# Performance work log

Measured on AMD Instinct MI355X. Metric: run time of the kernel, lower is better.

Reference implementation:

```python
import jax, jax.numpy as jnp
import numpy as np

N, D, C = 2048, 192, 100000
S, M = 30.0, 0.2

def setup_inputs() -> dict:
    key = jax.random.key(0)
    k1, k2, k3 = jax.random.split(key, 3)
    x = jax.random.normal(k1, (N, D), dtype=jnp.float32)
    W = jax.random.normal(k2, (C, D), dtype=jnp.float32) * 0.05
    label = jax.random.randint(k3, (N,), 0, C, dtype=jnp.int64)
    return {"x": x, "W": W, "label": label}

def reference(x, W, label):
    # NOTE: the original torch code's weight-normalization loop is a no-op
    # (it rebinds the local name W, never mutating the parameter), so W is
    # intentionally NOT normalized here; only x is.
    xn = x / jnp.linalg.norm(x, axis=1, keepdims=True)          # [N, D]
    wf = jnp.einsum("nd,cd->nc", xn, W)                          # [N, C]
    tgt = jnp.take_along_axis(wf, label[:, None], axis=1)[:, 0]  # [N]
    numer = S * (tgt - M)                                        # margin-adjusted target logit
    logits = S * wf
    # replace the label column with the margin-adjusted numerator so that
    # logsumexp(logits) == log(exp(numer) + sum_{j!=y} exp(s*wf[:,j]))
    logits = logits.at[jnp.arange(N), label].set(numer)
    L = numer - jax.nn.logsumexp(logits, axis=1)                 # [N]
    return -jnp.mean(L)
```

## Files before the change

kernel.cpp:

```cpp
#include <hip/hip_runtime.h>
#include <stdint.h>


constexpr int N  = 2048;
constexpr int D  = 192;
constexpr int C  = 100000;
constexpr int KT = D / 32;
constexpr int TILE = 512;
constexpr int RT16 = C / 16;
constexpr int TPG = 12;
constexpr int CX = 523;
constexpr int RY = 16;
constexpr int NT16 = CX * TPG;
constexpr float PHANTOM = (float)(NT16 * 16 - C);

#define S_SCALE 30.0f
#define MARGIN  0.2f
#define S_LOG2E 43.2808512266689f

using short8 = __attribute__((ext_vector_type(8))) short;
using f32x4  = __attribute__((ext_vector_type(4))) float;

typedef __attribute__((address_space(1))) const void GV;
typedef __attribute__((address_space(3))) void LV;

__device__ inline unsigned short f2bf(float f) {
  unsigned int u = __float_as_uint(f);
  u += 0x7fffu + ((u >> 16) & 1u);
  return (unsigned short)(u >> 16);
}

__device__ inline int pack_idx(int r, int k) {
  return ((r >> 4) * KT + (k >> 5)) * TILE + (((k >> 3) & 3) * 16 + (r & 15)) * 8 + (k & 7);
}

__device__ inline float row_sum16(float v) {
  int x;
  x = __float_as_int(v);
  v += __int_as_float(__builtin_amdgcn_update_dpp(0, x, 0x128, 0xF, 0xF, true));
  x = __float_as_int(v);
  v += __int_as_float(__builtin_amdgcn_update_dpp(0, x, 0x124, 0xF, 0xF, true));
  x = __float_as_int(v);
  v += __int_as_float(__builtin_amdgcn_update_dpp(0, x, 0x04E, 0xF, 0xF, true));
  x = __float_as_int(v);
  v += __int_as_float(__builtin_amdgcn_update_dpp(0, x, 0x0B1, 0xF, 0xF, true));
  return v;
}

__global__ __launch_bounds__(256) void prep_x(const float* __restrict__ x,
                                              unsigned short* __restrict__ xnb) {
  const int row  = blockIdx.x * 4 + (threadIdx.x >> 6);
  const int lane = threadIdx.x & 63;
  const float* xr = x + (size_t)row * D;
  float v0 = xr[lane], v1 = xr[lane + 64], v2 = xr[lane + 128];
  float ss = v0 * v0 + v1 * v1 + v2 * v2;
#pragma unroll
  for (int off = 32; off > 0; off >>= 1) ss += __shfl_xor(ss, off, 64);
  const float inv = rsqrtf(ss) * S_LOG2E;
  xnb[pack_idx(row, lane)]       = f2bf(v0 * inv);
  xnb[pack_idx(row, lane + 64)]  = f2bf(v1 * inv);
  xnb[pack_idx(row, lane + 128)] = f2bf(v2 * inv);
}

__global__ __launch_bounds__(256) void prep_w(const float* __restrict__ W,
                                              unsigned short* __restrict__ Wb) {
  const int t16  = blockIdx.x * 4 + (threadIdx.x >> 6);
  const int lane = threadIdx.x & 63;
  const int m = lane & 15, q = lane >> 4;
  unsigned short* dst = Wb + (size_t)t16 * KT * TILE + lane * 8;
  if (t16 < RT16) {
    const float* src = W + (size_t)(t16 * 16 + m) * D + q * 8;
#pragma unroll
    for (int ks = 0; ks < KT; ++ks) {
      const float4* s4 = (const float4*)(src + ks * 32);
      float4 f0 = s4[0], f1 = s4[1];
      short8 hv;
      hv[0] = (short)f2bf(f0.x); hv[1] = (short)f2bf(f0.y);
      hv[2] = (short)f2bf(f0.z); hv[3] = (short)f2bf(f0.w);
      hv[4] = (short)f2bf(f1.x); hv[5] = (short)f2bf(f1.y);
      hv[6] = (short)f2bf(f1.z); hv[7] = (short)f2bf(f1.w);
      *(short8*)(dst + (size_t)ks * TILE) = hv;
    }
  } else {
    const short8 z = {0, 0, 0, 0, 0, 0, 0, 0};
#pragma unroll
    for (int ks = 0; ks < KT; ++ks) *(short8*)(dst + (size_t)ks * TILE) = z;
  }
}

__global__ __launch_bounds__(256, 3) void gemm_lse(
    const unsigned short* __restrict__ xnb,
    const unsigned short* __restrict__ Wb,
    float* __restrict__ partial) {
  __shared__ alignas(16) unsigned short As[8 * KT * TILE];
  __shared__ alignas(16) float rs_lds[4][128];

  const int tid = threadIdx.x;
  const int bid = blockIdx.x;
  const int cx = bid >> 4, ry = bid & 15;

  const unsigned short* slab = xnb + (size_t)(ry * 8) * KT * TILE;
#pragma unroll
  for (int i = 0; i < 12; ++i) {
    const int chunk = tid + i * 256;
    __builtin_amdgcn_global_load_lds(
        (GV*)((const char*)slab + (size_t)chunk * 16),
        (LV*)((char*)As + (size_t)chunk * 16), 16, 0, 0);
  }

  const int lane = tid & 63, wave = tid >> 6;
  const int m = lane & 15, quad = lane >> 4;

  short8 breg[3][KT];
#pragma unroll
  for (int tc = 0; tc < 3; ++tc)
#pragma unroll
    for (int ks = 0; ks < KT; ++ks)
      breg[tc][ks] = *(const short8*)(
          Wb + (size_t)((cx * TPG + wave * 3 + tc) * KT + ks) * TILE + lane * 8);

  __syncthreads();

  const f32x4 zero4 = {0.0f, 0.0f, 0.0f, 0.0f};

  for (int rs = 0; rs < 2; ++rs) {
    f32x4 acc[4][3];
#pragma unroll
    for (int a = 0; a < 4; ++a)
#pragma unroll
      for (int b = 0; b < 3; ++b) acc[a][b] = zero4;

#pragma unroll
    for (int ks = 0; ks < KT; ++ks) {
      short8 af[4];
#pragma unroll
      for (int tr = 0; tr < 4; ++tr)
        af[tr] = *(const short8*)(
            &As[((rs * 4 + tr) * KT + ks) * TILE + lane * 8]);
#pragma unroll
      for (int tr = 0; tr < 4; ++tr)
#pragma unroll
        for (int tc = 0; tc < 3; ++tc)
          acc[tr][tc] = __builtin_amdgcn_mfma_f32_16x16x32_bf16(
              af[tr], breg[tc][ks], acc[tr][tc], 0, 0, 0);
    }

#pragma unroll
    for (int tr = 0; tr < 4; ++tr) {
      float rv0 = 0.f, rv1 = 0.f, rv2 = 0.f, rv3 = 0.f;
#pragma unroll
      for (int tc = 0; tc < 3; ++tc) {
        rv0 += __builtin_amdgcn_exp2f(acc[tr][tc][0]);
        rv1 += __builtin_amdgcn_exp2f(acc[tr][tc][1]);
        rv2 += __builtin_amdgcn_exp2f(acc[tr][tc][2]);
        rv3 += __builtin_amdgcn_exp2f(acc[tr][tc][3]);
      }
      rv0 = row_sum16(rv0);
      rv1 = row_sum16(rv1);
      rv2 = row_sum16(rv2);
      rv3 = row_sum16(rv3);
      if (m == 0) {
        float4 v = make_float4(rv0, rv1, rv2, rv3);
        *(float4*)(&rs_lds[wave][rs * 64 + tr * 16 + quad * 4]) = v;
      }
    }
  }

  __syncthreads();
  if (tid < 128) {
    const float s = rs_lds[0][tid] + rs_lds[1][tid] + rs_lds[2][tid] + rs_lds[3][tid];
    partial[(size_t)cx * N + ry * 128 + tid] = s;
  }
}

__global__ __launch_bounds__(256) void finalize_rows(
    const float* __restrict__ x, const float* __restrict__ W,
    const int* __restrict__ label, const float* __restrict__ partial,
    float* __restrict__ Lrow) {
  const int row  = blockIdx.x * 4 + (threadIdx.x >> 6);
  const int lane = threadIdx.x & 63;
  const float* xr = x + (size_t)row * D;
  float v0 = xr[lane], v1 = xr[lane + 64], v2 = xr[lane + 128];
  float ss = v0 * v0 + v1 * v1 + v2 * v2;
  const int lab = label[row];
  const float* wr = W + (size_t)lab * D;
  float d = v0 * wr[lane] + v1 * wr[lane + 64] + v2 * wr[lane + 128];
  float p = 0.0f;
  for (int s = lane; s < CX; s += 64) p += partial[(size_t)s * N + row];
#pragma unroll
  for (int off = 32; off > 0; off >>= 1) {
    ss += __shfl_xor(ss, off, 64);
    d  += __shfl_xor(d,  off, 64);
    p  += __shfl_xor(p,  off, 64);
  }
  if (lane == 0) {
    const float tgt   = d * rsqrtf(ss);
    const float numer = S_SCALE * (tgt - MARGIN);
    const float se = p - PHANTOM - __expf(S_SCALE * tgt) + __expf(numer);
    Lrow[row] = numer - logf(se);
  }
}

__global__ __launch_bounds__(256) void reduce_loss(const float* __restrict__ Lrow,
                                                   float* __restrict__ out) {
  const int tid = threadIdx.x;
  float s = 0.0f;
  for (int i = tid; i < N; i += 256) s += Lrow[i];
#pragma unroll
  for (int off = 32; off > 0; off >>= 1) s += __shfl_xor(s, off, 64);
  __shared__ float part[4];
  if ((tid & 63) == 0) part[tid >> 6] = s;
  __syncthreads();
  if (tid == 0) out[0] = -(part[0] + part[1] + part[2] + part[3]) / (float)N;
}

extern "C" void kernel_launch(void* const* d_in, const int* in_sizes, int n_in,
                              void* d_out, int out_size, void* d_ws, size_t ws_size,
                              hipStream_t stream) {
  const float* x     = (const float*)d_in[0];
  const float* W     = (const float*)d_in[1];
  const int*   label = (const int*)d_in[2];
  float*       out   = (float*)d_out;

  char* ws = (char*)d_ws;
  size_t off = 0;
  unsigned short* xnb = (unsigned short*)(ws + off); off += (size_t)N * D * 2;
  unsigned short* Wb  = (unsigned short*)(ws + off); off += (size_t)NT16 * KT * TILE * 2;
  float* partial = (float*)(ws + off); off += (size_t)CX * N * 4;
  float* Lrow    = (float*)(ws + off);

  prep_x<<<N / 4, 256, 0, stream>>>(x, xnb);
  prep_w<<<NT16 / 4, 256, 0, stream>>>(W, Wb);

  gemm_lse<<<CX * RY, 256, 0, stream>>>(xnb, Wb, partial);

  finalize_rows<<<N / 4, 256, 0, stream>>>(x, W, label, partial, Lrow);
  reduce_loss<<<1, 256, 0, stream>>>(Lrow, out);
}
```

Measured before the change: 214.5 us.

## Double-buffer x bands in GEMM-LSE, merge prep kernels, fuse final reduction

Each gemm_lse block now covers 256 rows in four bands of 64 instead of 128 rows. That halves the number of blocks that reload the same W tiles into registers. The next x band is streamed into a second LDS buffer while the current band is being multiplied. The two prep kernels are merged into one launch, which also zeroes the output. The separate reduce kernel is replaced by per-block atomicAdd in finalize_rows. This trades fewer launches and less W reloading for fewer, longer blocks (1/8 of the grid is now per-cx), a larger LDS footprint, and an order-dependent float atomic sum.

```diff
diff --git a/kernel.cpp b/kernel.cpp
--- a/kernel.cpp
+++ b/kernel.cpp
@@ -10,9 +10,12 @@
 constexpr int RT16 = C / 16;
 constexpr int TPG = 12;
 constexpr int CX = 523;
-constexpr int RY = 16;
 constexpr int NT16 = CX * TPG;
 constexpr float PHANTOM = (float)(NT16 * 16 - C);
+constexpr int BANDS = 4;
+constexpr int RYB = N / (64 * BANDS);
+constexpr int BUF = 4 * KT * TILE;
+constexpr int NXB = N / 4;
 
 #define S_SCALE 30.0f
 #define MARGIN  0.2f
@@ -47,44 +50,47 @@
   return v;
 }
 
-__global__ __launch_bounds__(256) void prep_x(const float* __restrict__ x,
-                                              unsigned short* __restrict__ xnb) {
-  const int row  = blockIdx.x * 4 + (threadIdx.x >> 6);
+__global__ __launch_bounds__(256) void prep_all(
+    const float* __restrict__ x, const float* __restrict__ W,
+    unsigned short* __restrict__ xnb, unsigned short* __restrict__ Wb,
+    float* __restrict__ out) {
+  const int bid  = blockIdx.x;
   const int lane = threadIdx.x & 63;
-  const float* xr = x + (size_t)row * D;
-  float v0 = xr[lane], v1 = xr[lane + 64], v2 = xr[lane + 128];
-  float ss = v0 * v0 + v1 * v1 + v2 * v2;
-#pragma unroll
-  for (int off = 32; off > 0; off >>= 1) ss += __shfl_xor(ss, off, 64);
-  const float inv = rsqrtf(ss) * S_LOG2E;
-  xnb[pack_idx(row, lane)]       = f2bf(v0 * inv);
-  xnb[pack_idx(row, lane + 64)]  = f2bf(v1 * inv);
-  xnb[pack_idx(row, lane + 128)] = f2bf(v2 * inv);
-}
-
-__global__ __launch_bounds__(256) void prep_w(const float* __restrict__ W,
-                                              unsigned short* __restrict__ Wb) {
-  const int t16  = blockIdx.x * 4 + (threadIdx.x >> 6);
-  const int lane = threadIdx.x & 63;
-  const int m = lane & 15, q = lane >> 4;
-  unsigned short* dst = Wb + (size_t)t16 * KT * TILE + lane * 8;
-  if (t16 < RT16) {
-    const float* src = W + (size_t)(t16 * 16 + m) * D + q * 8;
-#pragma unroll
-    for (int ks = 0; ks < KT; ++ks) {
-      const float4* s4 = (const float4*)(src + ks * 32);
-      float4 f0 = s4[0], f1 = s4[1];
-      short8 hv;
-      hv[0] = (short)f2bf(f0.x); hv[1] = (short)f2bf(f0.y);
-      hv[2] = (short)f2bf(f0.z); hv[3] = (short)f2bf(f0.w);
-      hv[4] = (short)f2bf(f1.x); hv[5] = (short)f2bf(f1.y);
-      hv[6] = (short)f2bf(f1.z); hv[7] = (short)f2bf(f1.w);
-      *(short8*)(dst + (size_t)ks * TILE) = hv;
-    }
+  if (bid == 0 && threadIdx.x == 0) out[0] = 0.0f;
+
+  if (bid < NXB) {
+    const int row = bid * 4 + (threadIdx.x >> 6);
+    const float* xr = x + (size_t)row * D;
+    float v0 = xr[lane], v1 = xr[lane + 64], v2 = xr[lane + 128];
+    float ss = v0 * v0 + v1 * v1 + v2 * v2;
+#pragma unroll
+    for (int off = 32; off > 0; off >>= 1) ss += __shfl_xor(ss, off, 64);
+    const float inv = rsqrtf(ss) * S_LOG2E;
+    xnb[pack_idx(row, lane)]       = f2bf(v0 * inv);
+    xnb[pack_idx(row, lane + 64)]  = f2bf(v1 * inv);
+    xnb[pack_idx(row, lane + 128)] = f2bf(v2 * inv);
   } else {
-    const short8 z = {0, 0, 0, 0, 0, 0, 0, 0};
-#pragma unroll
-    for (int ks = 0; ks < KT; ++ks) *(short8*)(dst + (size_t)ks * TILE) = z;
+    const int t16 = (bid - NXB) * 4 + (threadIdx.x >> 6);
+    const int m = lane & 15, q = lane >> 4;
+    unsigned short* dst = Wb + (size_t)t16 * KT * TILE + lane * 8;
+    if (t16 < RT16) {
+      const float* src = W + (size_t)(t16 * 16 + m) * D + q * 8;
+#pragma unroll
+      for (int ks = 0; ks < KT; ++ks) {
+        const float4* s4 = (const float4*)(src + ks * 32);
+        float4 f0 = s4[0], f1 = s4[1];
+        short8 hv;
+        hv[0] = (short)f2bf(f0.x); hv[1] = (short)f2bf(f0.y);
+        hv[2] = (short)f2bf(f0.z); hv[3] = (short)f2bf(f0.w);
+        hv[4] = (short)f2bf(f1.x); hv[5] = (short)f2bf(f1.y);
+        hv[6] = (short)f2bf(f1.z); hv[7] = (short)f2bf(f1.w);
+        *(short8*)(dst + (size_t)ks * TILE) = hv;
+      }
+    } else {
+      const short8 z = {0, 0, 0, 0, 0, 0, 0, 0};
+#pragma unroll
+      for (int ks = 0; ks < KT; ++ks) *(short8*)(dst + (size_t)ks * TILE) = z;
+    }
   }
 }
 
@@ -92,20 +98,22 @@
     const unsigned short* __restrict__ xnb,
     const unsigned short* __restrict__ Wb,
     float* __restrict__ partial) {
-  __shared__ alignas(16) unsigned short As[8 * KT * TILE];
-  __shared__ alignas(16) float rs_lds[4][128];
+  __shared__ alignas(16) unsigned short As[2 * BUF];
+  __shared__ alignas(16) float rs_lds[4][256];
 
   const int tid = threadIdx.x;
   const int bid = blockIdx.x;
-  const int cx = bid >> 4, ry = bid & 15;
-
-  const unsigned short* slab = xnb + (size_t)(ry * 8) * KT * TILE;
-#pragma unroll
-  for (int i = 0; i < 12; ++i) {
-    const int chunk = tid + i * 256;
-    __builtin_amdgcn_global_load_lds(
-        (GV*)((const char*)slab + (size_t)chunk * 16),
-        (LV*)((char*)As + (size_t)chunk * 16), 16, 0, 0);
+  const int cx = bid >> 3, ry = bid & 7;
+
+  {
+    const unsigned short* slab = xnb + (size_t)(ry * BANDS) * BUF;
+#pragma unroll
+    for (int i = 0; i < 6; ++i) {
+      const int chunk = tid + i * 256;
+      __builtin_amdgcn_global_load_lds(
+          (GV*)((const char*)slab + (size_t)chunk * 16),
+          (LV*)((char*)As + (size_t)chunk * 16), 16, 0, 0);
+    }
   }
 
   const int lane = tid & 63, wave = tid >> 6;
@@ -119,24 +127,37 @@
       breg[tc][ks] = *(const short8*)(
           Wb + (size_t)((cx * TPG + wave * 3 + tc) * KT + ks) * TILE + lane * 8);
 
-  __syncthreads();
-
   const f32x4 zero4 = {0.0f, 0.0f, 0.0f, 0.0f};
 
-  for (int rs = 0; rs < 2; ++rs) {
+  for (int b = 0; b < BANDS; ++b) {
+    __syncthreads();
+
+    if (b + 1 < BANDS) {
+      const unsigned short* slab = xnb + (size_t)(ry * BANDS + b + 1) * BUF;
+      char* dst = (char*)&As[((b + 1) & 1) * BUF];
+#pragma unroll
+      for (int i = 0; i < 6; ++i) {
+        const int chunk = tid + i * 256;
+        __builtin_amdgcn_global_load_lds(
+            (GV*)((const char*)slab + (size_t)chunk * 16),
+            (LV*)(dst + (size_t)chunk * 16), 16, 0, 0);
+      }
+    }
+
+    const unsigned short* Ab = &As[(b & 1) * BUF];
+
     f32x4 acc[4][3];
 #pragma unroll
     for (int a = 0; a < 4; ++a)
 #pragma unroll
-      for (int b = 0; b < 3; ++b) acc[a][b] = zero4;
+      for (int c = 0; c < 3; ++c) acc[a][c] = zero4;
 
 #pragma unroll
     for (int ks = 0; ks < KT; ++ks) {
       short8 af[4];
 #pragma unroll
       for (int tr = 0; tr < 4; ++tr)
-        af[tr] = *(const short8*)(
-            &As[((rs * 4 + tr) * KT + ks) * TILE + lane * 8]);
+        af[tr] = *(const short8*)(&Ab[(tr * KT + ks) * TILE + lane * 8]);
 #pragma unroll
       for (int tr = 0; tr < 4; ++tr)
 #pragma unroll
@@ -161,22 +182,22 @@
       rv3 = row_sum16(rv3);
       if (m == 0) {
         float4 v = make_float4(rv0, rv1, rv2, rv3);
-        *(float4*)(&rs_lds[wave][rs * 64 + tr * 16 + quad * 4]) = v;
+        *(float4*)(&rs_lds[wave][b * 64 + tr * 16 + quad * 4]) = v;
       }
     }
   }
 
   __syncthreads();
-  if (tid < 128) {
+  if (tid < 256) {
     const float s = rs_lds[0][tid] + rs_lds[1][tid] + rs_lds[2][tid] + rs_lds[3][tid];
-    partial[(size_t)cx * N + ry * 128 + tid] = s;
+    partial[(size_t)cx * N + ry * 256 + tid] = s;
   }
 }
 
 __global__ __launch_bounds__(256) void finalize_rows(
     const float* __restrict__ x, const float* __restrict__ W,
     const int* __restrict__ label, const float* __restrict__ partial,
-    float* __restrict__ Lrow) {
+    float* __restrict__ out) {
   const int row  = blockIdx.x * 4 + (threadIdx.x >> 6);
   const int lane = threadIdx.x & 63;
   const float* xr = x + (size_t)row * D;
@@ -193,25 +214,18 @@
     d  += __shfl_xor(d,  off, 64);
     p  += __shfl_xor(p,  off, 64);
   }
+  __shared__ float part[4];
   if (lane == 0) {
     const float tgt   = d * rsqrtf(ss);
     const float numer = S_SCALE * (tgt - MARGIN);
     const float se = p - PHANTOM - __expf(S_SCALE * tgt) + __expf(numer);
-    Lrow[row] = numer - logf(se);
-  }
-}
-
-__global__ __launch_bounds__(256) void reduce_loss(const float* __restrict__ Lrow,
-                                                   float* __restrict__ out) {
-  const int tid = threadIdx.x;
-  float s = 0.0f;
-  for (int i = tid; i < N; i += 256) s += Lrow[i];
-#pragma unroll
-  for (int off = 32; off > 0; off >>= 1) s += __shfl_xor(s, off, 64);
-  __shared__ float part[4];
-  if ((tid & 63) == 0) part[tid >> 6] = s;
+    part[threadIdx.x >> 6] = numer - logf(se);
+  }
   __syncthreads();
-  if (tid == 0) out[0] = -(part[0] + part[1] + part[2] + part[3]) / (float)N;
+  if (threadIdx.x == 0) {
+    const float blocksum = part[0] + part[1] + part[2] + part[3];
+    atomicAdd(out, -blocksum * (1.0f / (float)N));
+  }
 }
 
 extern "C" void kernel_launch(void* const* d_in, const int* in_sizes, int n_in,
@@ -227,13 +241,10 @@
   unsigned short* xnb = (unsigned short*)(ws + off); off += (size_t)N * D * 2;
   unsigned short* Wb  = (unsigned short*)(ws + off); off += (size_t)NT16 * KT * TILE * 2;
   float* partial = (float*)(ws + off); off += (size_t)CX * N * 4;
-  float* Lrow    = (float*)(ws + off);
-
-  prep_x<<<N / 4, 256, 0, stream>>>(x, xnb);
-  prep_w<<<NT16 / 4, 256, 0, stream>>>(W, Wb);
-
-  gemm_lse<<<CX * RY, 256, 0, stream>>>(xnb, Wb, partial);
-
-  finalize_rows<<<N / 4, 256, 0, stream>>>(x, W, label, partial, Lrow);
-  reduce_loss<<<1, 256, 0, stream>>>(Lrow, out);
-}
+
+  prep_all<<<NXB + NT16 / 4, 256, 0, stream>>>(x, W, xnb, Wb, out);
+
+  gemm_lse<<<CX * RYB, 256, 0, stream>>>(xnb, Wb, partial);
+
+  finalize_rows<<<N / 4, 256, 0, stream>>>(x, W, label, partial, out);
+}
```

Result: no change. 212.0 us (-1.2%).
